# Optimization experiments

Measured on AMD Instinct MI355X. Metric: run time of the kernel, lower is better.

The kernel has to match this reference:

```python
import jax, jax.numpy as jnp
import numpy as np

N_NODES = 100000
N_EDGES = 1600000
D_IN = 64
D_OUT = 64
ALPHA = 0.5


def setup_inputs() -> dict:
    key = jax.random.key(0)
    k_x, k_ei, k_w, k_ws, k_bs, k_wd, k_bd = jax.random.split(key, 7)
    x = jax.random.normal(k_x, (N_NODES, D_IN), dtype=jnp.float32)
    edge_index = jax.random.randint(k_ei, (2, N_EDGES), 0, N_NODES, dtype=jnp.int64)
    edge_weight = jax.random.uniform(k_w, (N_EDGES,), dtype=jnp.float32)
    # torch Linear init: uniform(-1/sqrt(fan_in), 1/sqrt(fan_in))
    bound = 1.0 / np.sqrt(D_IN)
    W_src = jax.random.uniform(k_ws, (D_OUT, D_IN), minval=-bound, maxval=bound, dtype=jnp.float32)
    b_src = jax.random.uniform(k_bs, (D_OUT,), minval=-bound, maxval=bound, dtype=jnp.float32)
    W_dst = jax.random.uniform(k_wd, (D_OUT, D_IN), minval=-bound, maxval=bound, dtype=jnp.float32)
    b_dst = jax.random.uniform(k_bd, (D_OUT,), minval=-bound, maxval=bound, dtype=jnp.float32)
    return {"x": x, "edge_index": edge_index, "edge_weight": edge_weight,
            "W_src": W_src, "b_src": b_src, "W_dst": W_dst, "b_dst": b_dst}


def _dir_norm_spmm(row, col, w, x, n):
    """Compute (D_out^{-1/2} A D_in^{-1/2}) @ x for A with entries (row, col, w)."""
    out_deg = jax.ops.segment_sum(w, row, num_segments=n)  # row sums (dim=1)
    in_deg = jax.ops.segment_sum(w, col, num_segments=n)   # col sums (dim=0)
    d_out = jnp.where(out_deg > 0, out_deg ** -0.5, 0.0)
    d_in = jnp.where(in_deg > 0, in_deg ** -0.5, 0.0)
    w_norm = w * d_out[row] * d_in[col]                    # [E]
    # SpMM: out[i] = sum_{e: row_e = i} w_norm_e * x[col_e]
    return jax.ops.segment_sum(w_norm[:, None] * x[col], row, num_segments=n)


def reference(x, edge_index, edge_weight, W_src, b_src, W_dst, b_dst):
    row, col = edge_index[0], edge_index[1]
    n = x.shape[0]
    agg_fwd = _dir_norm_spmm(row, col, edge_weight, x, n)   # adj_norm @ x
    agg_bwd = _dir_norm_spmm(col, row, edge_weight, x, n)   # adj_t_norm @ x
    out = ALPHA * (agg_fwd @ W_src.T + b_src) + (1.0 - ALPHA) * (agg_bwd @ W_dst.T + b_dst)
    return out
```

## Files before the change

kernel.cpp:

```cpp
#include <hip/hip_runtime.h>

#define D 64
#define ALPHA 0.5f
#define FXSCALE 16777216.f
#define CE 2048
#define BSH 9
#define BN 512
#define CAP 9216

typedef unsigned long long u64;
typedef unsigned short u16;
typedef unsigned int u32;
typedef float f32x4 __attribute__((ext_vector_type(4)));

static __device__ __forceinline__ u16 f2bf(float f) {
    unsigned u = __float_as_uint(f);
    unsigned r = (u + 0x7fffu + ((u >> 16) & 1u)) >> 16;
    return (u16)r;
}
static __device__ __forceinline__ float bf2f(u16 h) {
    return __uint_as_float(((unsigned)h) << 16);
}
static __device__ __forceinline__ float dinv_of_fx(u32 fx) {
    float s = (float)fx * (1.f / FXSCALE);
    return (s > 0.f) ? rsqrtf(s) : 0.f;
}

__global__ __launch_bounds__(512)
void p3_transform_kernel(const int* __restrict__ row, const int* __restrict__ col,
                         const float* __restrict__ w, u32* __restrict__ cursor,
                         u64* __restrict__ ent,
                         const float* __restrict__ x,
                         const float* __restrict__ Ws, const float* __restrict__ Wd,
                         u16* __restrict__ y1, u16* __restrict__ y2,
                         int N, int E, int NCH, int NBUCK, int NT, int total_blocks) {
    __shared__ u64 smem[6432];
    int b = blockIdx.x;
    int t = threadIdx.x;
    int t_before = (int)(((long long)b * NT) / total_blocks);
    bool is_t = (int)(((long long)(b + 1) * NT) / total_blocks) > t_before;

    if (!is_t) {
        int ch = b - t_before;
        u64* ebuf   = smem;
        u16* ebkt   = (u16*)(smem + 4096);
        u32* hcnt   = (u32*)(smem + 5120);
        u32* hstart = (u32*)(smem + 5376);
        u32* hoff   = (u32*)(smem + 5632);
        int* s      = (int*)(smem + 5888);
        u32* hbase  = (u32*)(smem + 6144);
        hcnt[t] = 0;
        __syncthreads();
        int e0 = ch * CE, e1 = min(E, e0 + CE);
        for (int e = e0 + t; e < e1; e += 512) {
            atomicAdd(&hcnt[(u32)row[e] >> BSH], 1u);
            atomicAdd(&hcnt[(u32)(N + col[e]) >> BSH], 1u);
        }
        __syncthreads();
        int v = (int)hcnt[t];
        s[t] = v;
        __syncthreads();
        for (int off = 1; off < 512; off <<= 1) {
            int u = (t >= off) ? s[t - off] : 0;
            __syncthreads();
            s[t] += u;
            __syncthreads();
        }
        hstart[t] = (u32)(s[t] - v);
        hoff[t]   = (u32)(s[t] - v);
        u32 myb = 0;
        if (t < NBUCK && v > 0) myb = atomicAdd(&cursor[t], (u32)v);
        hbase[t] = myb;
        __syncthreads();
        for (int e = e0 + t; e < e1; e += 512) {
            int r = row[e], c = col[e];
            u32 wb = __float_as_uint(w[e]);
            u32 b1 = (u32)r >> BSH;
            u64 q1 = ((u64)wb << 32) | ((u32)c << BSH) | ((u32)r & (BN - 1));
            u32 p1 = atomicAdd(&hoff[b1], 1u);
            ebuf[p1] = q1; ebkt[p1] = (u16)b1;
            u32 d2 = (u32)(N + c);
            u32 b2 = d2 >> BSH;
            u64 q2 = ((u64)wb << 32) | ((u32)r << BSH) | (d2 & (BN - 1));
            u32 p2 = atomicAdd(&hoff[b2], 1u);
            ebuf[p2] = q2; ebkt[p2] = (u16)b2;
        }
        __syncthreads();
        int nent = 2 * (e1 - e0);
        for (int p = t; p < nent; p += 512) {
            u32 bb = ebkt[p];
            u32 local = hbase[bb] + (u32)p - hstart[bb];
            if (local < CAP)
                ent[(size_t)bb * CAP + local] = ebuf[p];
        }
        return;
    }

    float* xs  = (float*)smem;
    float* Wt1 = xs + 64 * 65;
    float* Wt2 = Wt1 + 64 * 68;
    for (int i = t; i < 4096; i += 512) {
        int o = i >> 6, k = i & 63;
        Wt1[k * 68 + o] = Ws[i];
        Wt2[k * 68 + o] = Wd[i];
    }
    int r0 = t_before * 64;
    for (int i = t; i < 4096; i += 512) {
        int r = i >> 6, k = i & 63;
        int gr = r0 + r;
        xs[r * 65 + k] = (gr < N) ? x[(size_t)gr * D + k] : 0.f;
    }
    __syncthreads();
    int ro = t >> 4, co = t & 15;
    float a1[2][4] = {}, a2[2][4] = {};
#pragma unroll 4
    for (int k = 0; k < 64; ++k) {
        float v0 = xs[(ro * 2 + 0) * 65 + k];
        float v1 = xs[(ro * 2 + 1) * 65 + k];
        float4 b1 = *(const float4*)&Wt1[k * 68 + co * 4];
        float4 b2 = *(const float4*)&Wt2[k * 68 + co * 4];
        a1[0][0] += v0 * b1.x; a1[0][1] += v0 * b1.y; a1[0][2] += v0 * b1.z; a1[0][3] += v0 * b1.w;
        a1[1][0] += v1 * b1.x; a1[1][1] += v1 * b1.y; a1[1][2] += v1 * b1.z; a1[1][3] += v1 * b1.w;
        a2[0][0] += v0 * b2.x; a2[0][1] += v0 * b2.y; a2[0][2] += v0 * b2.z; a2[0][3] += v0 * b2.w;
        a2[1][0] += v1 * b2.x; a2[1][1] += v1 * b2.y; a2[1][2] += v1 * b2.z; a2[1][3] += v1 * b2.w;
    }
#pragma unroll
    for (int i = 0; i < 2; ++i) {
        int gr = r0 + ro * 2 + i;
        if (gr < N) {
            ushort4 o1, o2;
            o1.x = f2bf(a1[i][0] * ALPHA); o1.y = f2bf(a1[i][1] * ALPHA);
            o1.z = f2bf(a1[i][2] * ALPHA); o1.w = f2bf(a1[i][3] * ALPHA);
            o2.x = f2bf(a2[i][0] * (1.f - ALPHA)); o2.y = f2bf(a2[i][1] * (1.f - ALPHA));
            o2.z = f2bf(a2[i][2] * (1.f - ALPHA)); o2.w = f2bf(a2[i][3] * (1.f - ALPHA));
            *(ushort4*)&y1[(size_t)gr * D + co * 4] = o1;
            *(ushort4*)&y2[(size_t)gr * D + co * 4] = o2;
        }
    }
}

__global__ void p4_build_kernel(const u64* __restrict__ ent, const u32* __restrict__ cursor,
                                float* __restrict__ dinv, int2* __restrict__ ptr2,
                                float2* __restrict__ edata,
                                int L, int NBUCK) {
    __shared__ u32 cnt[512], fx[512], pstart[512], pfill[512];
    __shared__ int s[512];
    int t = threadIdx.x, b = blockIdx.x;
    int base0 = b * CAP;
    int nE = min((int)cursor[b], CAP);
    cnt[t] = 0; fx[t] = 0;
    __syncthreads();
    for (int i = t; i < nE; i += 512) {
        u64 q = ent[(size_t)base0 + i];
        u32 dlo = (u32)q & (BN - 1);
        float wv = __uint_as_float((u32)(q >> 32));
        atomicAdd(&cnt[dlo], 1u);
        atomicAdd(&fx[dlo], (u32)__float2uint_rn(wv * FXSCALE));
    }
    __syncthreads();
    int v = (int)cnt[t];
    s[t] = v;
    __syncthreads();
    for (int off = 1; off < 512; off <<= 1) {
        int u = (t >= off) ? s[t - off] : 0;
        __syncthreads();
        s[t] += u;
        __syncthreads();
    }
    pstart[t] = (u32)(s[t] - v);
    pfill[t]  = (u32)(s[t] - v);
    int node = b * BN + t;
    if (node < L) {
        dinv[node] = dinv_of_fx(fx[t]);
        int st = base0 + (int)pstart[t];
        ptr2[node] = make_int2(st, st + v);
    }
    __syncthreads();
    for (int i = t; i < nE; i += 512) {
        u64 q = ent[(size_t)base0 + i];
        u32 dlo = (u32)q & (BN - 1);
        u32 src = ((u32)q) >> BSH;
        float wv = __uint_as_float((u32)(q >> 32));
        u32 pos = atomicAdd(&pfill[dlo], 1u);
        edata[(size_t)base0 + pos] = make_float2(__int_as_float((int)src), wv);
    }
}

__global__ void gather_csr_kernel(const int2* __restrict__ ptr2, const float* __restrict__ dinv,
                                  const float2* __restrict__ ed,
                                  const u16* __restrict__ y1, const u16* __restrict__ y2,
                                  const float* __restrict__ b_src, const float* __restrict__ b_dst,
                                  float* __restrict__ out, int N) {
    int tid = threadIdx.x;
    int lane = tid & 63;
    int node = blockIdx.x * (blockDim.x >> 6) + (tid >> 6);
    if (node >= N) return;
    int g  = lane >> 4;
    int fl = lane & 15;

    int2 pf = ptr2[node];
    int2 pb = ptr2[N + node];
    int ef = pf.x, ef1 = pf.y;
    int eb = pb.x, eb1 = pb.y;
    const float* __restrict__ dsf = dinv + N;
    const float* __restrict__ dsb = dinv;

    float f0 = 0.f, f1 = 0.f, f2 = 0.f, f3 = 0.f;
    float b0 = 0.f, b1 = 0.f, b2 = 0.f, b3 = 0.f;

    while (ef < ef1 || eb < eb1) {
        if (ef < ef1) {
            int ea = ef + g, ex = ef + 4 + g, ea2 = ef + 8 + g, ex2 = ef + 12 + g;
            float2 da = (ea  < ef1) ? ed[ea]  : make_float2(__int_as_float(0), 0.f);
            float2 db = (ex  < ef1) ? ed[ex]  : make_float2(__int_as_float(0), 0.f);
            float2 dc = (ea2 < ef1) ? ed[ea2] : make_float2(__int_as_float(0), 0.f);
            float2 de = (ex2 < ef1) ? ed[ex2] : make_float2(__int_as_float(0), 0.f);
            int sa = __float_as_int(da.x), sb = __float_as_int(db.x);
            int sc = __float_as_int(dc.x), se = __float_as_int(de.x);
            float wa = da.y * dsf[sa], wb = db.y * dsf[sb];
            float wc = dc.y * dsf[sc], we = de.y * dsf[se];
            u64 qa = *(const u64*)(y1 + (((size_t)sa) << 6) + (fl << 2));
            u64 qb = *(const u64*)(y1 + (((size_t)sb) << 6) + (fl << 2));
            u64 qc = *(const u64*)(y1 + (((size_t)sc) << 6) + (fl << 2));
            u64 qe = *(const u64*)(y1 + (((size_t)se) << 6) + (fl << 2));
            f0 += wa * bf2f((u16)qa)         + wb * bf2f((u16)qb)
                + wc * bf2f((u16)qc)         + we * bf2f((u16)qe);
            f1 += wa * bf2f((u16)(qa >> 16)) + wb * bf2f((u16)(qb >> 16))
                + wc * bf2f((u16)(qc >> 16)) + we * bf2f((u16)(qe >> 16));
            f2 += wa * bf2f((u16)(qa >> 32)) + wb * bf2f((u16)(qb >> 32))
                + wc * bf2f((u16)(qc >> 32)) + we * bf2f((u16)(qe >> 32));
            f3 += wa * bf2f((u16)(qa >> 48)) + wb * bf2f((u16)(qb >> 48))
                + wc * bf2f((u16)(qc >> 48)) + we * bf2f((u16)(qe >> 48));
            ef += 16;
        }
        if (eb < eb1) {
            int ea = eb + g, ex = eb + 4 + g, ea2 = eb + 8 + g, ex2 = eb + 12 + g;
            float2 da = (ea  < eb1) ? ed[ea]  : make_float2(__int_as_float(0), 0.f);
            float2 db = (ex  < eb1) ? ed[ex]  : make_float2(__int_as_float(0), 0.f);
            float2 dc = (ea2 < eb1) ? ed[ea2] : make_float2(__int_as_float(0), 0.f);
            float2 de = (ex2 < eb1) ? ed[ex2] : make_float2(__int_as_float(0), 0.f);
            int sa = __float_as_int(da.x), sb = __float_as_int(db.x);
            int sc = __float_as_int(dc.x), se = __float_as_int(de.x);
            float wa = da.y * dsb[sa], wb = db.y * dsb[sb];
            float wc = dc.y * dsb[sc], we = de.y * dsb[se];
            u64 qa = *(const u64*)(y2 + (((size_t)sa) << 6) + (fl << 2));
            u64 qb = *(const u64*)(y2 + (((size_t)sb) << 6) + (fl << 2));
            u64 qc = *(const u64*)(y2 + (((size_t)sc) << 6) + (fl << 2));
            u64 qe = *(const u64*)(y2 + (((size_t)se) << 6) + (fl << 2));
            b0 += wa * bf2f((u16)qa)         + wb * bf2f((u16)qb)
                + wc * bf2f((u16)qc)         + we * bf2f((u16)qe);
            b1 += wa * bf2f((u16)(qa >> 16)) + wb * bf2f((u16)(qb >> 16))
                + wc * bf2f((u16)(qc >> 16)) + we * bf2f((u16)(qe >> 16));
            b2 += wa * bf2f((u16)(qa >> 32)) + wb * bf2f((u16)(qb >> 32))
                + wc * bf2f((u16)(qc >> 32)) + we * bf2f((u16)(qe >> 32));
            b3 += wa * bf2f((u16)(qa >> 48)) + wb * bf2f((u16)(qb >> 48))
                + wc * bf2f((u16)(qc >> 48)) + we * bf2f((u16)(qe >> 48));
            eb += 16;
        }
    }
    float dout = dinv[node], din = dinv[N + node];
    float v0 = f0 * dout + b0 * din;
    float v1 = f1 * dout + b1 * din;
    float v2 = f2 * dout + b2 * din;
    float v3 = f3 * dout + b3 * din;
    v0 += __shfl_xor(v0, 16); v0 += __shfl_xor(v0, 32);
    v1 += __shfl_xor(v1, 16); v1 += __shfl_xor(v1, 32);
    v2 += __shfl_xor(v2, 16); v2 += __shfl_xor(v2, 32);
    v3 += __shfl_xor(v3, 16); v3 += __shfl_xor(v3, 32);
    if (g == 0) {
        float4 bs = *(const float4*)&b_src[fl << 2];
        float4 bd = *(const float4*)&b_dst[fl << 2];
        f32x4 o;
        o.x = v0 + ALPHA * bs.x + (1.f - ALPHA) * bd.x;
        o.y = v1 + ALPHA * bs.y + (1.f - ALPHA) * bd.y;
        o.z = v2 + ALPHA * bs.z + (1.f - ALPHA) * bd.z;
        o.w = v3 + ALPHA * bs.w + (1.f - ALPHA) * bd.w;
        __builtin_nontemporal_store(o, (f32x4*)&out[((size_t)node << 6) + (fl << 2)]);
    }
}

extern "C" void kernel_launch(void* const* d_in, const int* in_sizes, int n_in,
                              void* d_out, int out_size, void* d_ws, size_t ws_size,
                              hipStream_t stream) {
    const float* x     = (const float*)d_in[0];
    const int*   ei    = (const int*)d_in[1];
    const float* w     = (const float*)d_in[2];
    const float* W_src = (const float*)d_in[3];
    const float* b_src = (const float*)d_in[4];
    const float* W_dst = (const float*)d_in[5];
    const float* b_dst = (const float*)d_in[6];
    float* out = (float*)d_out;

    const int N = in_sizes[0] / D;
    const int E = in_sizes[2];
    const int* row = ei;
    const int* col = ei + E;
    const int L = 2 * N;
    const int NCH   = (E + CE - 1) / CE;
    const int NBUCK = (L + BN - 1) >> BSH;
    const int NT    = (N + 63) / 64;

    char* base = (char*)d_ws;
    size_t o = 0;
    auto take = [&](size_t b) { char* p = base + o; o = (o + b + 63) & ~(size_t)63; return p; };
    u32*    cursor = (u32*)take((size_t)NBUCK * 4);
    u64*    ent    = (u64*)take((size_t)NBUCK * CAP * 8);
    float*  dinv   = (float*)take((size_t)L * 4);
    int2*   ptr2   = (int2*)take((size_t)L * 8);
    u16*    y1     = (u16*)take((size_t)N * D * 2);
    u16*    y2     = (u16*)take((size_t)N * D * 2);
    float2* edata  = (float2*)take((size_t)NBUCK * CAP * 8);

    hipMemsetAsync(cursor, 0, (size_t)NBUCK * 4, stream);
    p3_transform_kernel<<<NCH + NT, 512, 0, stream>>>(row, col, w, cursor, ent,
                                                      x, W_src, W_dst, y1, y2,
                                                      N, E, NCH, NBUCK, NT, NCH + NT);
    p4_build_kernel<<<NBUCK, 512, 0, stream>>>(ent, cursor, dinv, ptr2, edata, L, NBUCK);
    gather_csr_kernel<<<(N + 3) / 4, 256, 0, stream>>>(ptr2, dinv, edata, y1, y2,
                                                       b_src, b_dst, out, N);
}
```

Baseline: 203.9 us.

## Co-schedule dense transform with CSR build instead of edge bucketing; nontemporal edge loads

Moves the dense x·W transform blocks out of the edge-bucketing kernel and into the CSR-build kernel, so the transform runs alongside the per-bucket build rather than the scatter sort. This rebalances block mixes across the two launches and gives the sort kernel its own static shared memory. The gather kernel now reads edge records as 64-bit nontemporal loads to keep the streaming edge data from displacing cached feature rows. How much this helps depends on which phase had more idle capacity, and NBUCK is small, so the build kernel may become dominated by transform blocks.

```diff
diff --git a/kernel.cpp b/kernel.cpp
--- a/kernel.cpp
+++ b/kernel.cpp
@@ -27,13 +27,68 @@
 }
 
 __global__ __launch_bounds__(512)
-void p3_transform_kernel(const int* __restrict__ row, const int* __restrict__ col,
-                         const float* __restrict__ w, u32* __restrict__ cursor,
-                         u64* __restrict__ ent,
+void p3_sort_kernel(const int* __restrict__ row, const int* __restrict__ col,
+                    const float* __restrict__ w, u32* __restrict__ cursor,
+                    u64* __restrict__ ent, int N, int E, int NBUCK) {
+    __shared__ u64 ebuf[4096];
+    __shared__ u16 ebkt[4096];
+    __shared__ u32 hcnt[512], hstart[512], hoff[512], hbase[512];
+    __shared__ int s[512];
+    int t = threadIdx.x, ch = blockIdx.x;
+    hcnt[t] = 0;
+    __syncthreads();
+    int e0 = ch * CE, e1 = min(E, e0 + CE);
+    for (int e = e0 + t; e < e1; e += 512) {
+        atomicAdd(&hcnt[(u32)row[e] >> BSH], 1u);
+        atomicAdd(&hcnt[(u32)(N + col[e]) >> BSH], 1u);
+    }
+    __syncthreads();
+    int v = (int)hcnt[t];
+    s[t] = v;
+    __syncthreads();
+    for (int off = 1; off < 512; off <<= 1) {
+        int u = (t >= off) ? s[t - off] : 0;
+        __syncthreads();
+        s[t] += u;
+        __syncthreads();
+    }
+    hstart[t] = (u32)(s[t] - v);
+    hoff[t]   = (u32)(s[t] - v);
+    u32 myb = 0;
+    if (t < NBUCK && v > 0) myb = atomicAdd(&cursor[t], (u32)v);
+    hbase[t] = myb;
+    __syncthreads();
+    for (int e = e0 + t; e < e1; e += 512) {
+        int r = row[e], c = col[e];
+        u32 wb = __float_as_uint(w[e]);
+        u32 b1 = (u32)r >> BSH;
+        u64 q1 = ((u64)wb << 32) | ((u32)c << BSH) | ((u32)r & (BN - 1));
+        u32 p1 = atomicAdd(&hoff[b1], 1u);
+        ebuf[p1] = q1; ebkt[p1] = (u16)b1;
+        u32 d2 = (u32)(N + c);
+        u32 b2 = d2 >> BSH;
+        u64 q2 = ((u64)wb << 32) | ((u32)r << BSH) | (d2 & (BN - 1));
+        u32 p2 = atomicAdd(&hoff[b2], 1u);
+        ebuf[p2] = q2; ebkt[p2] = (u16)b2;
+    }
+    __syncthreads();
+    int nent = 2 * (e1 - e0);
+    for (int p = t; p < nent; p += 512) {
+        u32 bb = ebkt[p];
+        u32 local = hbase[bb] + (u32)p - hstart[bb];
+        if (local < CAP)
+            ent[(size_t)bb * CAP + local] = ebuf[p];
+    }
+}
+
+__global__ __launch_bounds__(512)
+void p4_transform_kernel(const u64* __restrict__ ent, const u32* __restrict__ cursor,
+                         float* __restrict__ dinv, int2* __restrict__ ptr2,
+                         float2* __restrict__ edata,
                          const float* __restrict__ x,
                          const float* __restrict__ Ws, const float* __restrict__ Wd,
                          u16* __restrict__ y1, u16* __restrict__ y2,
-                         int N, int E, int NCH, int NBUCK, int NT, int total_blocks) {
+                         int N, int L, int NBUCK, int NT, int total_blocks) {
     __shared__ u64 smem[6432];
     int b = blockIdx.x;
     int t = threadIdx.x;
@@ -41,23 +96,25 @@
     bool is_t = (int)(((long long)(b + 1) * NT) / total_blocks) > t_before;
 
     if (!is_t) {
-        int ch = b - t_before;
-        u64* ebuf   = smem;
-        u16* ebkt   = (u16*)(smem + 4096);
-        u32* hcnt   = (u32*)(smem + 5120);
-        u32* hstart = (u32*)(smem + 5376);
-        u32* hoff   = (u32*)(smem + 5632);
-        int* s      = (int*)(smem + 5888);
-        u32* hbase  = (u32*)(smem + 6144);
-        hcnt[t] = 0;
-        __syncthreads();
-        int e0 = ch * CE, e1 = min(E, e0 + CE);
-        for (int e = e0 + t; e < e1; e += 512) {
-            atomicAdd(&hcnt[(u32)row[e] >> BSH], 1u);
-            atomicAdd(&hcnt[(u32)(N + col[e]) >> BSH], 1u);
-        }
-        __syncthreads();
-        int v = (int)hcnt[t];
+        int bk = b - t_before;
+        u32* cnt    = (u32*)smem;
+        u32* fx     = (u32*)(smem + 256);
+        u32* pstart = (u32*)(smem + 512);
+        u32* pfill  = (u32*)(smem + 768);
+        int* s      = (int*)(smem + 1024);
+        int base0 = bk * CAP;
+        int nE = min((int)cursor[bk], CAP);
+        cnt[t] = 0; fx[t] = 0;
+        __syncthreads();
+        for (int i = t; i < nE; i += 512) {
+            u64 q = ent[(size_t)base0 + i];
+            u32 dlo = (u32)q & (BN - 1);
+            float wv = __uint_as_float((u32)(q >> 32));
+            atomicAdd(&cnt[dlo], 1u);
+            atomicAdd(&fx[dlo], (u32)__float2uint_rn(wv * FXSCALE));
+        }
+        __syncthreads();
+        int v = (int)cnt[t];
         s[t] = v;
         __syncthreads();
         for (int off = 1; off < 512; off <<= 1) {
@@ -66,32 +123,22 @@
             s[t] += u;
             __syncthreads();
         }
-        hstart[t] = (u32)(s[t] - v);
-        hoff[t]   = (u32)(s[t] - v);
-        u32 myb = 0;
-        if (t < NBUCK && v > 0) myb = atomicAdd(&cursor[t], (u32)v);
-        hbase[t] = myb;
-        __syncthreads();
-        for (int e = e0 + t; e < e1; e += 512) {
-            int r = row[e], c = col[e];
-            u32 wb = __float_as_uint(w[e]);
-            u32 b1 = (u32)r >> BSH;
-            u64 q1 = ((u64)wb << 32) | ((u32)c << BSH) | ((u32)r & (BN - 1));
-            u32 p1 = atomicAdd(&hoff[b1], 1u);
-            ebuf[p1] = q1; ebkt[p1] = (u16)b1;
-            u32 d2 = (u32)(N + c);
-            u32 b2 = d2 >> BSH;
-            u64 q2 = ((u64)wb << 32) | ((u32)r << BSH) | (d2 & (BN - 1));
-            u32 p2 = atomicAdd(&hoff[b2], 1u);
-            ebuf[p2] = q2; ebkt[p2] = (u16)b2;
-        }
-        __syncthreads();
-        int nent = 2 * (e1 - e0);
-        for (int p = t; p < nent; p += 512) {
-            u32 bb = ebkt[p];
-            u32 local = hbase[bb] + (u32)p - hstart[bb];
-            if (local < CAP)
-                ent[(size_t)bb * CAP + local] = ebuf[p];
+        pstart[t] = (u32)(s[t] - v);
+        pfill[t]  = (u32)(s[t] - v);
+        int node = bk * BN + t;
+        if (node < L) {
+            dinv[node] = dinv_of_fx(fx[t]);
+            int st = base0 + (int)pstart[t];
+            ptr2[node] = make_int2(st, st + v);
+        }
+        __syncthreads();
+        for (int i = t; i < nE; i += 512) {
+            u64 q = ent[(size_t)base0 + i];
+            u32 dlo = (u32)q & (BN - 1);
+            u32 src = ((u32)q) >> BSH;
+            float wv = __uint_as_float((u32)(q >> 32));
+            u32 pos = atomicAdd(&pfill[dlo], 1u);
+            edata[(size_t)base0 + pos] = make_float2(__int_as_float((int)src), wv);
         }
         return;
     }
@@ -139,53 +186,6 @@
     }
 }
 
-__global__ void p4_build_kernel(const u64* __restrict__ ent, const u32* __restrict__ cursor,
-                                float* __restrict__ dinv, int2* __restrict__ ptr2,
-                                float2* __restrict__ edata,
-                                int L, int NBUCK) {
-    __shared__ u32 cnt[512], fx[512], pstart[512], pfill[512];
-    __shared__ int s[512];
-    int t = threadIdx.x, b = blockIdx.x;
-    int base0 = b * CAP;
-    int nE = min((int)cursor[b], CAP);
-    cnt[t] = 0; fx[t] = 0;
-    __syncthreads();
-    for (int i = t; i < nE; i += 512) {
-        u64 q = ent[(size_t)base0 + i];
-        u32 dlo = (u32)q & (BN - 1);
-        float wv = __uint_as_float((u32)(q >> 32));
-        atomicAdd(&cnt[dlo], 1u);
-        atomicAdd(&fx[dlo], (u32)__float2uint_rn(wv * FXSCALE));
-    }
-    __syncthreads();
-    int v = (int)cnt[t];
-    s[t] = v;
-    __syncthreads();
-    for (int off = 1; off < 512; off <<= 1) {
-        int u = (t >= off) ? s[t - off] : 0;
-        __syncthreads();
-        s[t] += u;
-        __syncthreads();
-    }
-    pstart[t] = (u32)(s[t] - v);
-    pfill[t]  = (u32)(s[t] - v);
-    int node = b * BN + t;
-    if (node < L) {
-        dinv[node] = dinv_of_fx(fx[t]);
-        int st = base0 + (int)pstart[t];
-        ptr2[node] = make_int2(st, st + v);
-    }
-    __syncthreads();
-    for (int i = t; i < nE; i += 512) {
-        u64 q = ent[(size_t)base0 + i];
-        u32 dlo = (u32)q & (BN - 1);
-        u32 src = ((u32)q) >> BSH;
-        float wv = __uint_as_float((u32)(q >> 32));
-        u32 pos = atomicAdd(&pfill[dlo], 1u);
-        edata[(size_t)base0 + pos] = make_float2(__int_as_float((int)src), wv);
-    }
-}
-
 __global__ void gather_csr_kernel(const int2* __restrict__ ptr2, const float* __restrict__ dinv,
                                   const float2* __restrict__ ed,
                                   const u16* __restrict__ y1, const u16* __restrict__ y2,
@@ -204,6 +204,7 @@
     int eb = pb.x, eb1 = pb.y;
     const float* __restrict__ dsf = dinv + N;
     const float* __restrict__ dsb = dinv;
+    const u64* __restrict__ edq = (const u64*)ed;
 
     float f0 = 0.f, f1 = 0.f, f2 = 0.f, f3 = 0.f;
     float b0 = 0.f, b1 = 0.f, b2 = 0.f, b3 = 0.f;
@@ -211,14 +212,16 @@
     while (ef < ef1 || eb < eb1) {
         if (ef < ef1) {
             int ea = ef + g, ex = ef + 4 + g, ea2 = ef + 8 + g, ex2 = ef + 12 + g;
-            float2 da = (ea  < ef1) ? ed[ea]  : make_float2(__int_as_float(0), 0.f);
-            float2 db = (ex  < ef1) ? ed[ex]  : make_float2(__int_as_float(0), 0.f);
-            float2 dc = (ea2 < ef1) ? ed[ea2] : make_float2(__int_as_float(0), 0.f);
-            float2 de = (ex2 < ef1) ? ed[ex2] : make_float2(__int_as_float(0), 0.f);
-            int sa = __float_as_int(da.x), sb = __float_as_int(db.x);
-            int sc = __float_as_int(dc.x), se = __float_as_int(de.x);
-            float wa = da.y * dsf[sa], wb = db.y * dsf[sb];
-            float wc = dc.y * dsf[sc], we = de.y * dsf[se];
+            u64 qda = (ea  < ef1) ? __builtin_nontemporal_load(&edq[ea])  : 0ULL;
+            u64 qdb = (ex  < ef1) ? __builtin_nontemporal_load(&edq[ex])  : 0ULL;
+            u64 qdc = (ea2 < ef1) ? __builtin_nontemporal_load(&edq[ea2]) : 0ULL;
+            u64 qde = (ex2 < ef1) ? __builtin_nontemporal_load(&edq[ex2]) : 0ULL;
+            int sa = (int)(qda & 0xffffffffULL), sb = (int)(qdb & 0xffffffffULL);
+            int sc = (int)(qdc & 0xffffffffULL), se = (int)(qde & 0xffffffffULL);
+            float wa = __uint_as_float((u32)(qda >> 32)) * dsf[sa];
+            float wb = __uint_as_float((u32)(qdb >> 32)) * dsf[sb];
+            float wc = __uint_as_float((u32)(qdc >> 32)) * dsf[sc];
+            float we = __uint_as_float((u32)(qde >> 32)) * dsf[se];
             u64 qa = *(const u64*)(y1 + (((size_t)sa) << 6) + (fl << 2));
             u64 qb = *(const u64*)(y1 + (((size_t)sb) << 6) + (fl << 2));
             u64 qc = *(const u64*)(y1 + (((size_t)sc) << 6) + (fl << 2));
@@ -235,14 +238,16 @@
         }
         if (eb < eb1) {
             int ea = eb + g, ex = eb + 4 + g, ea2 = eb + 8 + g, ex2 = eb + 12 + g;
-            float2 da = (ea  < eb1) ? ed[ea]  : make_float2(__int_as_float(0), 0.f);
-            float2 db = (ex  < eb1) ? ed[ex]  : make_float2(__int_as_float(0), 0.f);
-            float2 dc = (ea2 < eb1) ? ed[ea2] : make_float2(__int_as_float(0), 0.f);
-            float2 de = (ex2 < eb1) ? ed[ex2] : make_float2(__int_as_float(0), 0.f);
-            int sa = __float_as_int(da.x), sb = __float_as_int(db.x);
-            int sc = __float_as_int(dc.x), se = __float_as_int(de.x);
-            float wa = da.y * dsb[sa], wb = db.y * dsb[sb];
-            float wc = dc.y * dsb[sc], we = de.y * dsb[se];
+            u64 qda = (ea  < eb1) ? __builtin_nontemporal_load(&edq[ea])  : 0ULL;
+            u64 qdb = (ex  < eb1) ? __builtin_nontemporal_load(&edq[ex])  : 0ULL;
+            u64 qdc = (ea2 < eb1) ? __builtin_nontemporal_load(&edq[ea2]) : 0ULL;
+            u64 qde = (ex2 < eb1) ? __builtin_nontemporal_load(&edq[ex2]) : 0ULL;
+            int sa = (int)(qda & 0xffffffffULL), sb = (int)(qdb & 0xffffffffULL);
+            int sc = (int)(qdc & 0xffffffffULL), se = (int)(qde & 0xffffffffULL);
+            float wa = __uint_as_float((u32)(qda >> 32)) * dsb[sa];
+            float wb = __uint_as_float((u32)(qdb >> 32)) * dsb[sb];
+            float wc = __uint_as_float((u32)(qdc >> 32)) * dsb[sc];
+            float we = __uint_as_float((u32)(qde >> 32)) * dsb[se];
             u64 qa = *(const u64*)(y2 + (((size_t)sa) << 6) + (fl << 2));
             u64 qb = *(const u64*)(y2 + (((size_t)sb) << 6) + (fl << 2));
             u64 qc = *(const u64*)(y2 + (((size_t)sc) << 6) + (fl << 2));
@@ -312,10 +317,10 @@
     float2* edata  = (float2*)take((size_t)NBUCK * CAP * 8);
 
     hipMemsetAsync(cursor, 0, (size_t)NBUCK * 4, stream);
-    p3_transform_kernel<<<NCH + NT, 512, 0, stream>>>(row, col, w, cursor, ent,
-                                                      x, W_src, W_dst, y1, y2,
-                                                      N, E, NCH, NBUCK, NT, NCH + NT);
-    p4_build_kernel<<<NBUCK, 512, 0, stream>>>(ent, cursor, dinv, ptr2, edata, L, NBUCK);
+    p3_sort_kernel<<<NCH, 512, 0, stream>>>(row, col, w, cursor, ent, N, E, NBUCK);
+    p4_transform_kernel<<<NBUCK + NT, 512, 0, stream>>>(ent, cursor, dinv, ptr2, edata,
+                                                        x, W_src, W_dst, y1, y2,
+                                                        N, L, NBUCK, NT, NBUCK + NT);
     gather_csr_kernel<<<(N + 3) / 4, 256, 0, stream>>>(ptr2, dinv, edata, y1, y2,
                                                        b_src, b_dst, out, N);
 }
```

Measured after the change: 216.6 us. 1.06x slower.
